# Kernel tuning notes

Hardware: AMD Instinct MI355X
Metric: run time of the kernel (lower is better)

Reference implementation:

```python
import jax, jax.numpy as jnp
import numpy as np

B, S, K, N = 4, 2048, 4096, 4096


def setup_inputs() -> dict:
    key = jax.random.key(0)
    kx, kw = jax.random.split(key)
    # int8 activations and weights in [-127, 127), matching torch.randint(-127,127,...)
    x = jax.random.randint(kx, (B, S, K), -127, 127, dtype=jnp.int32).astype(jnp.int8)
    weight = jax.random.randint(kw, (N, K), -127, 127, dtype=jnp.int32).astype(jnp.int8)
    bias = jnp.zeros((1, N), dtype=jnp.int32)
    out_scale = jnp.ones((), dtype=jnp.float32)
    bias_scale = jnp.ones((), dtype=jnp.float32)
    return {"x": x, "weight": weight, "bias": bias,
            "out_scale": out_scale, "bias_scale": bias_scale}


def reference(x, weight, bias, out_scale, bias_scale):
    # Flatten leading dims: [B, S, K] -> [M, K]
    x_shape = x.shape
    x2 = x.reshape(-1, x_shape[-1])
    acc = jax.lax.dot_general(
        x2, weight,
        dimension_numbers=(((1,), (1,)), ((), ())),
        preferred_element_type=jnp.int32,
    )  # [M, N] int32
    # Fused epilogue: y = round(out_scale * acc + bias_scale * bias) -> int32
    y = jnp.round(acc.astype(jnp.float32) * out_scale
                  + bias.astype(jnp.float32) * bias_scale).astype(jnp.int32)
    return y.reshape(*x_shape[:-1], -1)
```

## Files before the change

kernel.cpp:

```cpp
#include <hip/hip_runtime.h>
#include <stdint.h>


typedef int v4i __attribute__((ext_vector_type(4)));

#define BM 256
#define BN 256
#define BK 128
#define KK 4096
#define KT (KK / BK)

__global__ __launch_bounds__(256)
void pack_i32_to_i8(const v4i* __restrict__ src, int* __restrict__ dst, int n4) {
    int i = blockIdx.x * blockDim.x + threadIdx.x;
    if (i >= n4) return;
    v4i a = src[i];
    dst[i] = (a[0] & 0xff) | ((a[1] & 0xff) << 8) | ((a[2] & 0xff) << 16) | (a[3] << 24);
}

__device__ __forceinline__ void gld_lds16(const void* g, void* lds) {
    __builtin_amdgcn_global_load_lds(
        (const __attribute__((address_space(1))) unsigned int*)g,
        (__attribute__((address_space(3))) unsigned int*)lds,
        16, 0, 0);
}

#define MFMA_I8 __builtin_amdgcn_mfma_i32_16x16x64_i8
#define BARRIER() __builtin_amdgcn_s_barrier()
#define LGKM0() asm volatile("s_waitcnt lgkmcnt(0)" ::: "memory")
#define PRIO(x) __builtin_amdgcn_s_setprio(x)

__global__ __launch_bounds__(512, 2)
void w8a8_gemm_kernel(const int8_t* __restrict__ X,
                      const int8_t* __restrict__ W,
                      const int*    __restrict__ bias,
                      const float*  __restrict__ out_scale_p,
                      const float*  __restrict__ bias_scale_p,
                      int*          __restrict__ Y,
                      int M, int N)
{
    __shared__ __align__(16) int8_t sA[2 * BM * BK];
    __shared__ __align__(16) int8_t sB[2 * BN * BK];

    const int tid = threadIdx.x;

    const int nbx = N / BN;
    const int nby = M / BM;
    int bx, by;
    {
        const int wg = blockIdx.x;
        if (nbx == 16 && nby == 32) {
            const int x = wg & 7;
            const int k = wg >> 3;
            bx = ((x & 1) << 3) | (k & 7);
            by = ((x >> 1) << 3) | (k >> 3);
        } else { bx = wg % nbx; by = wg / nbx; }
    }
    const int bn = bx * BN;
    const int bm = by * BM;

    const float out_scale  = *out_scale_p;
    const float bias_scale = *bias_scale_p;

    const int8_t* Abase = X + (size_t)bm * KK;
    const int8_t* Bbase = W + (size_t)bn * KK;

    const int r0  = tid >> 3;
    const int j0  = tid & 7;
    const int sw  = (j0 ^ (r0 & 7)) << 4;
    const size_t gOff = (size_t)r0 * KK + sw;
    const int  lOff = tid << 4;

#define STAGE(gbase, lds, t, h) do {                                              \
        const int8_t* _g = (gbase) + (size_t)((h) * 128) * KK                     \
                                   + (size_t)(t) * BK + gOff;                     \
        int8_t* _l = (lds) + (((t) & 1) << 15) + ((h) << 14) + lOff;              \
        gld_lds16(_g,                  _l);                                       \
        gld_lds16(_g + (size_t)64 * KK, _l + 8192);                               \
    } while (0)

    const int w    = tid >> 6;
    const int l    = tid & 63;
    const int wmw  = w >> 2;
    const int wnw  = w & 3;
    const int tm   = l & 15;
    const int quad = l >> 4;
    const int s3   = tm & 7;
    const int xo0  = ( quad      ^ s3) << 4;
    const int xo1  = ((quad + 4) ^ s3) << 4;
    const int rowA = ((wmw << 7) + tm) << 7;
    const int rowB = ((wnw << 6) + tm) << 7;

    v4i acc[8][4];
    const v4i vz = {0, 0, 0, 0};
#pragma unroll
    for (int i = 0; i < 8; ++i)
#pragma unroll
        for (int j = 0; j < 4; ++j)
            acc[i][j] = vz;

    STAGE(Abase, sA, 0, 0); STAGE(Abase, sA, 0, 1);
    STAGE(Bbase, sB, 0, 0); STAGE(Bbase, sB, 0, 1);
    STAGE(Abase, sA, 1, 0); STAGE(Abase, sA, 1, 1);
    asm volatile("s_waitcnt vmcnt(4)" ::: "memory");
    BARRIER();

#pragma unroll 2
    for (int t = 0; t < KT; ++t) {
        const int bo = (t & 1) << 15;
        const int8_t* sAb = sA + bo;
        const int8_t* sBb = sB + bo;
        v4i aF[8][2], bL[2][2], bH[2][2];

#pragma unroll
        for (int i = 0; i < 4; ++i) {
            aF[i][0] = *(const v4i*)(sAb + rowA + i * 2048 + xo0);
            aF[i][1] = *(const v4i*)(sAb + rowA + i * 2048 + xo1);
        }
#pragma unroll
        for (int j = 0; j < 2; ++j) {
            bL[j][0] = *(const v4i*)(sBb + rowB + j * 2048 + xo0);
            bL[j][1] = *(const v4i*)(sBb + rowB + j * 2048 + xo1);
        }
        if (t + 1 < KT) STAGE(Bbase, sB, t + 1, 0);
        BARRIER();
        LGKM0();
        PRIO(1);
#pragma unroll
        for (int i = 0; i < 4; ++i)
#pragma unroll
            for (int j = 0; j < 2; ++j) {
                acc[i][j] = MFMA_I8(aF[i][0], bL[j][0], acc[i][j], 0, 0, 0);
                acc[i][j] = MFMA_I8(aF[i][1], bL[j][1], acc[i][j], 0, 0, 0);
            }
        PRIO(0);
        BARRIER();

#pragma unroll
        for (int i = 4; i < 8; ++i) {
            aF[i][0] = *(const v4i*)(sAb + rowA + i * 2048 + xo0);
            aF[i][1] = *(const v4i*)(sAb + rowA + i * 2048 + xo1);
        }
        if (t + 1 < KT) STAGE(Bbase, sB, t + 1, 1);
        BARRIER();
        LGKM0();
        PRIO(1);
#pragma unroll
        for (int i = 4; i < 8; ++i)
#pragma unroll
            for (int j = 0; j < 2; ++j) {
                acc[i][j] = MFMA_I8(aF[i][0], bL[j][0], acc[i][j], 0, 0, 0);
                acc[i][j] = MFMA_I8(aF[i][1], bL[j][1], acc[i][j], 0, 0, 0);
            }
        PRIO(0);
        BARRIER();

#pragma unroll
        for (int j = 0; j < 2; ++j) {
            bH[j][0] = *(const v4i*)(sBb + rowB + (j + 2) * 2048 + xo0);
            bH[j][1] = *(const v4i*)(sBb + rowB + (j + 2) * 2048 + xo1);
        }
        if (t + 2 < KT) STAGE(Abase, sA, t + 2, 0);
        BARRIER();
        LGKM0();
        PRIO(1);
#pragma unroll
        for (int i = 0; i < 4; ++i)
#pragma unroll
            for (int j = 0; j < 2; ++j) {
                acc[i][j + 2] = MFMA_I8(aF[i][0], bH[j][0], acc[i][j + 2], 0, 0, 0);
                acc[i][j + 2] = MFMA_I8(aF[i][1], bH[j][1], acc[i][j + 2], 0, 0, 0);
            }
        PRIO(0);
        BARRIER();

        if (t + 2 < KT) {
            STAGE(Abase, sA, t + 2, 1);
            asm volatile("s_waitcnt vmcnt(4)" ::: "memory");
        } else {
            asm volatile("s_waitcnt vmcnt(0)" ::: "memory");
        }
        BARRIER();
        PRIO(1);
#pragma unroll
        for (int i = 4; i < 8; ++i)
#pragma unroll
            for (int j = 0; j < 2; ++j) {
                acc[i][j + 2] = MFMA_I8(aF[i][0], bH[j][0], acc[i][j + 2], 0, 0, 0);
                acc[i][j + 2] = MFMA_I8(aF[i][1], bH[j][1], acc[i][j + 2], 0, 0, 0);
            }
        PRIO(0);
        BARRIER();
    }
#undef STAGE

#pragma unroll
    for (int j = 0; j < 4; ++j) {
        const int n = bn + (wnw << 6) + (j << 4) + tm;
        const float bb = (float)bias[n] * bias_scale;
#pragma unroll
        for (int i = 0; i < 8; ++i) {
            const int mb = bm + (wmw << 7) + (i << 4) + (quad << 2);
#pragma unroll
            for (int r = 0; r < 4; ++r) {
                const float v = (float)acc[i][j][r] * out_scale + bb;
                Y[(size_t)(mb + r) * N + n] = (int)rintf(v);
            }
        }
    }
}

extern "C" void kernel_launch(void* const* d_in, const int* in_sizes, int n_in,
                              void* d_out, int out_size, void* d_ws, size_t ws_size,
                              hipStream_t stream) {
    const int* x32 = (const int*)d_in[0];
    const int* w32 = (const int*)d_in[1];
    const int*    bias = (const int*)d_in[2];
    const float*  os   = (const float*)d_in[3];
    const float*  bs   = (const float*)d_in[4];
    int* out = (int*)d_out;

    const int K = KK;
    const int M = in_sizes[0] / K;
    const int N = in_sizes[1] / K;
    const int nx = in_sizes[0];
    const int nw = in_sizes[1];

    int8_t* x8 = (int8_t*)d_ws;
    int8_t* w8 = x8 + (size_t)nx;

    pack_i32_to_i8<<<dim3(nx / 4 / 256), dim3(256), 0, stream>>>((const v4i*)x32, (int*)x8, nx / 4);
    pack_i32_to_i8<<<dim3(nw / 4 / 256), dim3(256), 0, stream>>>((const v4i*)w32, (int*)w8, nw / 4);

    dim3 grid((N / BN) * (M / BM));
    dim3 block(512);
    hipLaunchKernelGGL(w8a8_gemm_kernel, grid, block, 0, stream,
                       x8, w8, bias, os, bs, out, M, N);
}
```

Before: 415.2 us.

## Restructure K-loop phases to split by k-half and prefetch A tiles first

Reorganizes the main loop so each of the four phases covers one k-half (xo0/xo1) across all four B column fragments, with 16 MFMAs per phase, instead of splitting by B column pairs. The prefetch order is swapped: the next A tile is staged in the first two phases and B is prefetched two tiles ahead, with the prologue changed to match. Fragment register use drops from aF[8][2] plus bL/bH to a0/a1/b0/b1, which may relieve VGPR pressure. The epilogue is reordered so the column loop is innermost per output row. The intent is a better LDS-read/compute interleave and fewer live registers, at the risk of new LDS hazards from the changed staging order.

```diff
diff --git a/kernel.cpp b/kernel.cpp
--- a/kernel.cpp
+++ b/kernel.cpp
@@ -101,7 +101,7 @@
 
     STAGE(Abase, sA, 0, 0); STAGE(Abase, sA, 0, 1);
     STAGE(Bbase, sB, 0, 0); STAGE(Bbase, sB, 0, 1);
-    STAGE(Abase, sA, 1, 0); STAGE(Abase, sA, 1, 1);
+    STAGE(Bbase, sB, 1, 0); STAGE(Bbase, sB, 1, 1);
     asm volatile("s_waitcnt vmcnt(4)" ::: "memory");
     BARRIER();
 
@@ -110,101 +110,95 @@
         const int bo = (t & 1) << 15;
         const int8_t* sAb = sA + bo;
         const int8_t* sBb = sB + bo;
-        v4i aF[8][2], bL[2][2], bH[2][2];
-
-#pragma unroll
-        for (int i = 0; i < 4; ++i) {
-            aF[i][0] = *(const v4i*)(sAb + rowA + i * 2048 + xo0);
-            aF[i][1] = *(const v4i*)(sAb + rowA + i * 2048 + xo1);
-        }
-#pragma unroll
-        for (int j = 0; j < 2; ++j) {
-            bL[j][0] = *(const v4i*)(sBb + rowB + j * 2048 + xo0);
-            bL[j][1] = *(const v4i*)(sBb + rowB + j * 2048 + xo1);
-        }
-        if (t + 1 < KT) STAGE(Bbase, sB, t + 1, 0);
-        BARRIER();
-        LGKM0();
-        PRIO(1);
-#pragma unroll
-        for (int i = 0; i < 4; ++i)
-#pragma unroll
-            for (int j = 0; j < 2; ++j) {
-                acc[i][j] = MFMA_I8(aF[i][0], bL[j][0], acc[i][j], 0, 0, 0);
-                acc[i][j] = MFMA_I8(aF[i][1], bL[j][1], acc[i][j], 0, 0, 0);
-            }
-        PRIO(0);
-        BARRIER();
-
-#pragma unroll
-        for (int i = 4; i < 8; ++i) {
-            aF[i][0] = *(const v4i*)(sAb + rowA + i * 2048 + xo0);
-            aF[i][1] = *(const v4i*)(sAb + rowA + i * 2048 + xo1);
-        }
-        if (t + 1 < KT) STAGE(Bbase, sB, t + 1, 1);
-        BARRIER();
-        LGKM0();
-        PRIO(1);
-#pragma unroll
-        for (int i = 4; i < 8; ++i)
-#pragma unroll
-            for (int j = 0; j < 2; ++j) {
-                acc[i][j] = MFMA_I8(aF[i][0], bL[j][0], acc[i][j], 0, 0, 0);
-                acc[i][j] = MFMA_I8(aF[i][1], bL[j][1], acc[i][j], 0, 0, 0);
-            }
-        PRIO(0);
-        BARRIER();
-
-#pragma unroll
-        for (int j = 0; j < 2; ++j) {
-            bH[j][0] = *(const v4i*)(sBb + rowB + (j + 2) * 2048 + xo0);
-            bH[j][1] = *(const v4i*)(sBb + rowB + (j + 2) * 2048 + xo1);
-        }
-        if (t + 2 < KT) STAGE(Abase, sA, t + 2, 0);
-        BARRIER();
-        LGKM0();
-        PRIO(1);
-#pragma unroll
-        for (int i = 0; i < 4; ++i)
-#pragma unroll
-            for (int j = 0; j < 2; ++j) {
-                acc[i][j + 2] = MFMA_I8(aF[i][0], bH[j][0], acc[i][j + 2], 0, 0, 0);
-                acc[i][j + 2] = MFMA_I8(aF[i][1], bH[j][1], acc[i][j + 2], 0, 0, 0);
-            }
-        PRIO(0);
-        BARRIER();
-
+        v4i a0[4], a1[4], b0[4], b1[4];
+
+#pragma unroll
+        for (int i = 0; i < 4; ++i)
+            a0[i] = *(const v4i*)(sAb + rowA + i * 2048 + xo0);
+#pragma unroll
+        for (int j = 0; j < 4; ++j)
+            b0[j] = *(const v4i*)(sBb + rowB + j * 2048 + xo0);
+        if (t + 1 < KT) STAGE(Abase, sA, t + 1, 0);
+        BARRIER();
+        LGKM0();
+        PRIO(1);
+#pragma unroll
+        for (int i = 0; i < 4; ++i)
+#pragma unroll
+            for (int j = 0; j < 4; ++j)
+                acc[i][j] = MFMA_I8(a0[i], b0[j], acc[i][j], 0, 0, 0);
+        PRIO(0);
+        BARRIER();
+
+#pragma unroll
+        for (int i = 0; i < 4; ++i)
+            a1[i] = *(const v4i*)(sAb + rowA + (i + 4) * 2048 + xo0);
+#pragma unroll
+        for (int j = 0; j < 4; ++j)
+            b1[j] = *(const v4i*)(sBb + rowB + j * 2048 + xo1);
+        if (t + 1 < KT) STAGE(Abase, sA, t + 1, 1);
+        BARRIER();
+        LGKM0();
+        PRIO(1);
+#pragma unroll
+        for (int i = 0; i < 4; ++i)
+#pragma unroll
+            for (int j = 0; j < 4; ++j)
+                acc[i + 4][j] = MFMA_I8(a1[i], b0[j], acc[i + 4][j], 0, 0, 0);
+        PRIO(0);
+        BARRIER();
+
+#pragma unroll
+        for (int i = 0; i < 4; ++i)
+            a0[i] = *(const v4i*)(sAb + rowA + i * 2048 + xo1);
+        if (t + 2 < KT) STAGE(Bbase, sB, t + 2, 0);
+        BARRIER();
+        LGKM0();
+        PRIO(1);
+#pragma unroll
+        for (int i = 0; i < 4; ++i)
+#pragma unroll
+            for (int j = 0; j < 4; ++j)
+                acc[i][j] = MFMA_I8(a0[i], b1[j], acc[i][j], 0, 0, 0);
+        PRIO(0);
+        BARRIER();
+
+#pragma unroll
+        for (int i = 0; i < 4; ++i)
+            a1[i] = *(const v4i*)(sAb + rowA + (i + 4) * 2048 + xo1);
         if (t + 2 < KT) {
-            STAGE(Abase, sA, t + 2, 1);
+            STAGE(Bbase, sB, t + 2, 1);
             asm volatile("s_waitcnt vmcnt(4)" ::: "memory");
         } else {
             asm volatile("s_waitcnt vmcnt(0)" ::: "memory");
         }
         BARRIER();
-        PRIO(1);
-#pragma unroll
-        for (int i = 4; i < 8; ++i)
-#pragma unroll
-            for (int j = 0; j < 2; ++j) {
-                acc[i][j + 2] = MFMA_I8(aF[i][0], bH[j][0], acc[i][j + 2], 0, 0, 0);
-                acc[i][j + 2] = MFMA_I8(aF[i][1], bH[j][1], acc[i][j + 2], 0, 0, 0);
-            }
+        LGKM0();
+        PRIO(1);
+#pragma unroll
+        for (int i = 0; i < 4; ++i)
+#pragma unroll
+            for (int j = 0; j < 4; ++j)
+                acc[i + 4][j] = MFMA_I8(a1[i], b1[j], acc[i + 4][j], 0, 0, 0);
         PRIO(0);
         BARRIER();
     }
 #undef STAGE
 
-#pragma unroll
-    for (int j = 0; j < 4; ++j) {
-        const int n = bn + (wnw << 6) + (j << 4) + tm;
-        const float bb = (float)bias[n] * bias_scale;
-#pragma unroll
-        for (int i = 0; i < 8; ++i) {
-            const int mb = bm + (wmw << 7) + (i << 4) + (quad << 2);
-#pragma unroll
-            for (int r = 0; r < 4; ++r) {
-                const float v = (float)acc[i][j][r] * out_scale + bb;
-                Y[(size_t)(mb + r) * N + n] = (int)rintf(v);
+    float bb[4];
+#pragma unroll
+    for (int j = 0; j < 4; ++j)
+        bb[j] = (float)bias[bn + (wnw << 6) + (j << 4) + tm] * bias_scale;
+#pragma unroll
+    for (int i = 0; i < 8; ++i) {
+        const int mb = bm + (wmw << 7) + (i << 4) + (quad << 2);
+#pragma unroll
+        for (int r = 0; r < 4; ++r) {
+            int* yrow = Y + (size_t)(mb + r) * N + bn + (wnw << 6) + tm;
+#pragma unroll
+            for (int j = 0; j < 4; ++j) {
+                const float v = (float)acc[i][j][r] * out_scale + bb[j];
+                yrow[j << 4] = (int)rintf(v);
             }
         }
     }
```

After: 385.3 us. 7.2% less time.
